# Kernel optimization log

Hardware: AMD Instinct MI355X
Metric: run time of the kernel (lower is better)

Reference implementation:

```python
import jax, jax.numpy as jnp
import numpy as np

IN_CH = 64
OUT_CH = 32
SCALE = 2
BLOCK = SCALE ** 3  # 8
N = 400000   # input sparse voxels (lines in pair_fwd)
M = 200000   # output sparse voxels


def setup_inputs() -> dict:
    key = jax.random.key(0)
    k1, k2, k3 = jax.random.split(key, 3)
    x_features = jax.random.normal(k1, (N, IN_CH), dtype=jnp.float32)
    # flat ParameterList: weights[i*BLOCK + j] is the (in_channels,) weight for
    # output channel i, kernel position j
    weights = jax.random.normal(k2, (BLOCK * OUT_CH, IN_CH), dtype=jnp.float32)
    # spconv pair_fwd: [kernel_volume, num_lines], -1 marks invalid mapping
    pair_fwd = jax.random.randint(k3, (BLOCK, N), -1, M)
    return {"x_features": x_features, "weights": weights,
            "pair_fwd": pair_fwd, "num_out": M}


def reference(x_features, weights, pair_fwd, num_out):
    block, n = pair_fwd.shape
    out_ch = weights.shape[0] // block
    # W[o, j, c] == weights_list[o*block + j]
    W = weights.reshape(out_ch, block, -1)
    # sequential VoxelShuffle then .view(-1) per block is identity on each
    # voxel's in_channels feature vector, so:
    # vals[j, n, o] = dot(W[o, j, :], x_features[n, :])
    vals = jnp.einsum('nc,ojc->jno', x_features, W)  # [block, N, out_ch]
    idx = pair_fwd.reshape(-1)                       # [block*N]
    # route invalid (-1) entries to a dummy trailing row
    safe = jnp.where(idx >= 0, idx, num_out)
    buf = jnp.zeros((num_out + 1, out_ch), dtype=vals.dtype)
    # original uses assignment (set) semantics into out_features
    buf = buf.at[safe].set(vals.reshape(block * n, out_ch))
    return buf[:num_out]
```

## Files before the change

kernel.cpp:

```cpp
#include <hip/hip_runtime.h>

#define IN_CH  64
#define OUT_CH 32
#define BLOCK  8

using short8 = __attribute__((ext_vector_type(8))) short;
using f32x4v = __attribute__((ext_vector_type(4))) float;


__global__ void k_prep(int4* __restrict__ argmax4, int n4, int* __restrict__ cur) {
    int i = blockIdx.x * 256 + threadIdx.x;
    if (i < 16) cur[i] = 0;
    if (i < n4) argmax4[i] = make_int4(-1, -1, -1, -1);
}

__global__ void k_scatter_range(const int* __restrict__ pair, int* __restrict__ argmax,
                                int N, int jhi, int jlo, int flip) {
    int n = blockIdx.x * 256 + threadIdx.x;
    if (n >= N) return;
    if (flip) n = N - 1 - n;
    for (int j = jhi; j >= jlo; --j) {
        int t = j * N + n;
        int m = pair[t];
        if (m >= 0 && argmax[m] < t)
            atomicMax(&argmax[m], t);
    }
}

__global__ void k_fill(const int* __restrict__ argmax, int* __restrict__ cur,
                       int* __restrict__ bm, int* __restrict__ bn, int M, int N) {
    __shared__ int h9[9];
    __shared__ int b9[9];
    if (threadIdx.x < 9) h9[threadIdx.x] = 0;
    __syncthreads();
    int m = blockIdx.x * 256 + threadIdx.x;
    int j = 9, n = 0, lo = 0;
    if (m < M) {
        int t = argmax[m];
        if (t >= 0) { j = (int)((unsigned)t / (unsigned)N); n = t - j * N; }
        else j = 8;
        lo = atomicAdd(&h9[j], 1);
    }
    __syncthreads();
    if (threadIdx.x < 9 && h9[threadIdx.x] > 0)
        b9[threadIdx.x] = atomicAdd(&cur[threadIdx.x], h9[threadIdx.x]);
    __syncthreads();
    if (m < M) {
        int pos = j * M + b9[j] + lo;
        bm[pos] = m;
        bn[pos] = n;
    }
}

__device__ __forceinline__ unsigned cvt_pk_bf16(float lo, float hi) {
    unsigned r;
    asm("v_cvt_pk_bf16_f32 %0, %1, %2" : "=v"(r) : "v"(lo), "v"(hi));
    return r;
}

__device__ __forceinline__ short8 pack8(float4 a, float4 b) {
    union { unsigned u[4]; short8 s; } p;
    p.u[0] = cvt_pk_bf16(a.x, a.y);
    p.u[1] = cvt_pk_bf16(a.z, a.w);
    p.u[2] = cvt_pk_bf16(b.x, b.y);
    p.u[3] = cvt_pk_bf16(b.z, b.w);
    return p.s;
}

__global__ __launch_bounds__(256, 4) void k_compute(
        const float* __restrict__ x, const float* __restrict__ w,
        const int* __restrict__ cnt, const int* __restrict__ bm,
        const int* __restrict__ bn, float* __restrict__ out, int M, int N) {
    const int lane = threadIdx.x & 63;
    const int r16  = lane & 15;
    const int kc   = lane >> 4;
    const int wv   = threadIdx.x >> 6;

    int T = blockIdx.x * 4 + wv;
    int j = 0, nrows = 0;
    for (; j < 9; ++j) {
        int c  = cnt[j];
        int nt = (c + 63) >> 6;
        if (T < nt) { nrows = min(64, c - T * 64); break; }
        T -= nt;
    }
    if (j >= 9) return;
    int base = j * M + T * 64;
    int jw = (j < 8) ? j : 0;

    short8 bf[2][2];
#pragma unroll
    for (int ot = 0; ot < 2; ++ot)
#pragma unroll
        for (int kk = 0; kk < 2; ++kk) {
            const float* wp = w + ((ot * 16 + r16) * BLOCK + jw) * IN_CH + kk * 32 + kc * 8;
            bf[ot][kk] = pack8(*(const float4*)wp, *(const float4*)(wp + 4));
        }

#pragma unroll
    for (int st = 0; st < 4; ++st) {
        if (st * 16 >= nrows) break;
        int lrow = st * 16 + r16;
        int n    = bn[base + ((lrow < nrows) ? lrow : 0)];
        const float* xp = x + (size_t)n * IN_CH + kc * 8;
        float4 x0 = *(const float4*)xp;
        float4 x1 = *(const float4*)(xp + 4);
        float4 x2 = *(const float4*)(xp + 32);
        float4 x3 = *(const float4*)(xp + 36);
        short8 a0 = pack8(x0, x1);
        short8 a1 = pack8(x2, x3);

        f32x4v acc0 = {0.f, 0.f, 0.f, 0.f};
        f32x4v acc1 = {0.f, 0.f, 0.f, 0.f};
        acc0 = __builtin_amdgcn_mfma_f32_16x16x32_bf16(a0, bf[0][0], acc0, 0, 0, 0);
        acc0 = __builtin_amdgcn_mfma_f32_16x16x32_bf16(a1, bf[0][1], acc0, 0, 0, 0);
        acc1 = __builtin_amdgcn_mfma_f32_16x16x32_bf16(a0, bf[1][0], acc1, 0, 0, 0);
        acc1 = __builtin_amdgcn_mfma_f32_16x16x32_bf16(a1, bf[1][1], acc1, 0, 0, 0);

        int4 m4 = *(const int4*)&bm[base + st * 16 + kc * 4];
        int ma[4] = {m4.x, m4.y, m4.z, m4.w};
#pragma unroll
        for (int q = 0; q < 4; ++q) {
            int grow = st * 16 + kc * 4 + q;
            if (grow < nrows) {
                size_t ro = (size_t)ma[q] * OUT_CH;
                float v0 = (j == 8) ? 0.f : acc0[q];
                float v1 = (j == 8) ? 0.f : acc1[q];
                out[ro + r16]      = v0;
                out[ro + 16 + r16] = v1;
            }
        }
    }
}

extern "C" void kernel_launch(void* const* d_in, const int* in_sizes, int n_in,
                              void* d_out, int out_size, void* d_ws, size_t ws_size,
                              hipStream_t stream) {
    const float* x    = (const float*)d_in[0];
    const float* w    = (const float*)d_in[1];
    const int*   pair = (const int*)d_in[2];
    int N = in_sizes[0] / IN_CH;
    int M = out_size / OUT_CH;

    char* ws     = (char*)d_ws;
    int*  cur    = (int*)ws;
    int*  argmax = (int*)(ws + 256);
    int*  bm     = (int*)(ws + 256 + (size_t)M * 4);
    int*  bn     = (int*)(ws + 256 + (size_t)M * 4 + (size_t)9 * M * 4);

    int n4 = M / 4;
    k_prep<<<(n4 + 255) / 256, 256, 0, stream>>>((int4*)argmax, n4, cur);

    int gN = (N + 255) / 256;
    k_scatter_range<<<gN, 256, 0, stream>>>(pair, argmax, N, 7, 7, 1);
    k_scatter_range<<<gN, 256, 0, stream>>>(pair, argmax, N, 6, 0, 0);

    k_fill<<<(M + 255) / 256, 256, 0, stream>>>(argmax, cur, bm, bn, M, N);

    int maxtiles = (M + 63) / 64 + 9;
    int blocks   = (maxtiles + 3) / 4;
    k_compute<<<blocks, 256, 0, stream>>>(x, w, cur, bm, bn, (float*)d_out, M, N);
}
```

Baseline: 91.30 us.

## Drop bucketing fill pass; compute directly per output row with masked per-kernel MFMAs

Removes the k_fill pass that bucketed output rows by kernel position, along with its bm/bn index arrays. The compute kernel now reads argmax per output row, decodes j and n, and runs MFMAs for every kernel position present in the wave, zero-masking rows that belong to other positions. All 8 weight slices are held in registers and the next x row is prefetched. The scatter kernels now read pair entries as int4 vectors. The change saves one launch plus the bm/bn writes and reads, and output stores become contiguous instead of scattered. In exchange it can issue up to 8x more MFMAs per tile, raises register pressure (launch bounds lowered to 2), and assumes N is divisible by 4.

```diff
diff --git a/kernel.cpp b/kernel.cpp
--- a/kernel.cpp
+++ b/kernel.cpp
@@ -8,47 +8,33 @@
 using f32x4v = __attribute__((ext_vector_type(4))) float;
 
 
-__global__ void k_prep(int4* __restrict__ argmax4, int n4, int* __restrict__ cur) {
+__global__ void k_prep(int4* __restrict__ argmax4, int n4) {
     int i = blockIdx.x * 256 + threadIdx.x;
-    if (i < 16) cur[i] = 0;
     if (i < n4) argmax4[i] = make_int4(-1, -1, -1, -1);
 }
 
-__global__ void k_scatter_range(const int* __restrict__ pair, int* __restrict__ argmax,
-                                int N, int jhi, int jlo, int flip) {
-    int n = blockIdx.x * 256 + threadIdx.x;
-    if (n >= N) return;
-    if (flip) n = N - 1 - n;
-    for (int j = jhi; j >= jlo; --j) {
-        int t = j * N + n;
-        int m = pair[t];
-        if (m >= 0 && argmax[m] < t)
-            atomicMax(&argmax[m], t);
-    }
+__global__ void k_scatter7(const int* __restrict__ pair, int* __restrict__ argmax, int N) {
+    int i = blockIdx.x * 256 + threadIdx.x;
+    int q = N / 4 - 1 - i;
+    if (q < 0) return;
+    int4 p = ((const int4*)(pair + 7 * N))[q];
+    int tb = 7 * N + q * 4;
+    if (p.w >= 0 && argmax[p.w] < tb + 3) atomicMax(&argmax[p.w], tb + 3);
+    if (p.z >= 0 && argmax[p.z] < tb + 2) atomicMax(&argmax[p.z], tb + 2);
+    if (p.y >= 0 && argmax[p.y] < tb + 1) atomicMax(&argmax[p.y], tb + 1);
+    if (p.x >= 0 && argmax[p.x] < tb)     atomicMax(&argmax[p.x], tb);
 }
 
-__global__ void k_fill(const int* __restrict__ argmax, int* __restrict__ cur,
-                       int* __restrict__ bm, int* __restrict__ bn, int M, int N) {
-    __shared__ int h9[9];
-    __shared__ int b9[9];
-    if (threadIdx.x < 9) h9[threadIdx.x] = 0;
-    __syncthreads();
-    int m = blockIdx.x * 256 + threadIdx.x;
-    int j = 9, n = 0, lo = 0;
-    if (m < M) {
-        int t = argmax[m];
-        if (t >= 0) { j = (int)((unsigned)t / (unsigned)N); n = t - j * N; }
-        else j = 8;
-        lo = atomicAdd(&h9[j], 1);
-    }
-    __syncthreads();
-    if (threadIdx.x < 9 && h9[threadIdx.x] > 0)
-        b9[threadIdx.x] = atomicAdd(&cur[threadIdx.x], h9[threadIdx.x]);
-    __syncthreads();
-    if (m < M) {
-        int pos = j * M + b9[j] + lo;
-        bm[pos] = m;
-        bn[pos] = n;
+__global__ void k_scatter_rest(const int* __restrict__ pair, int* __restrict__ argmax, int N) {
+    int i = blockIdx.x * 256 + threadIdx.x;
+    if (i >= N / 4) return;
+    for (int j = 6; j >= 0; --j) {
+        int4 p = ((const int4*)(pair + j * N))[i];
+        int tb = j * N + i * 4;
+        if (p.x >= 0 && argmax[p.x] < tb)     atomicMax(&argmax[p.x], tb);
+        if (p.y >= 0 && argmax[p.y] < tb + 1) atomicMax(&argmax[p.y], tb + 1);
+        if (p.z >= 0 && argmax[p.z] < tb + 2) atomicMax(&argmax[p.z], tb + 2);
+        if (p.w >= 0 && argmax[p.w] < tb + 3) atomicMax(&argmax[p.w], tb + 3);
     }
 }
 
@@ -67,67 +53,91 @@
     return p.s;
 }
 
-__global__ __launch_bounds__(256, 4) void k_compute(
+__global__ __launch_bounds__(256, 2) void k_compute(
         const float* __restrict__ x, const float* __restrict__ w,
-        const int* __restrict__ cnt, const int* __restrict__ bm,
-        const int* __restrict__ bn, float* __restrict__ out, int M, int N) {
+        const int* __restrict__ argmax, float* __restrict__ out,
+        int M, int N) {
     const int lane = threadIdx.x & 63;
     const int r16  = lane & 15;
     const int kc   = lane >> 4;
     const int wv   = threadIdx.x >> 6;
 
-    int T = blockIdx.x * 4 + wv;
-    int j = 0, nrows = 0;
-    for (; j < 9; ++j) {
-        int c  = cnt[j];
-        int nt = (c + 63) >> 6;
-        if (T < nt) { nrows = min(64, c - T * 64); break; }
-        T -= nt;
+    int base = (blockIdx.x * 4 + wv) * 64;
+    if (base >= M) return;
+
+    short8 bf[8][2][2];
+#pragma unroll
+    for (int j = 0; j < 8; ++j)
+#pragma unroll
+        for (int ot = 0; ot < 2; ++ot)
+#pragma unroll
+            for (int kk = 0; kk < 2; ++kk) {
+                const float* wp = w + ((ot * 16 + r16) * BLOCK + j) * IN_CH + kk * 32 + kc * 8;
+                bf[j][ot][kk] = pack8(*(const float4*)wp, *(const float4*)(wp + 4));
+            }
+
+    const int N1 = N, N2 = 2 * N, N4 = 4 * N;
+
+    int t_[4], j_[4], n_[4];
+#pragma unroll
+    for (int st = 0; st < 4; ++st) {
+        int row = base + st * 16 + r16;
+        t_[st] = (row < M) ? argmax[row] : -1;
     }
-    if (j >= 9) return;
-    int base = j * M + T * 64;
-    int jw = (j < 8) ? j : 0;
+#pragma unroll
+    for (int st = 0; st < 4; ++st) {
+        int v = t_[st], j = 0;
+        if (v >= N4) { j = 4;  v -= N4; }
+        if (v >= N2) { j += 2; v -= N2; }
+        if (v >= N1) { j += 1; v -= N1; }
+        bool ok = t_[st] >= 0;
+        j_[st] = ok ? j : 8;
+        n_[st] = ok ? v : 0;
+    }
 
-    short8 bf[2][2];
+    float4 xs[2][4];
+    {
+        const float* xp = x + (size_t)n_[0] * IN_CH + kc * 8;
+        xs[0][0] = *(const float4*)xp;       xs[0][1] = *(const float4*)(xp + 4);
+        xs[0][2] = *(const float4*)(xp + 32); xs[0][3] = *(const float4*)(xp + 36);
+    }
+
 #pragma unroll
-    for (int ot = 0; ot < 2; ++ot)
+    for (int st = 0; st < 4; ++st) {
+        const int cur = st & 1;
+        if (st < 3) {
+            const float* xp = x + (size_t)n_[st + 1] * IN_CH + kc * 8;
+            xs[cur ^ 1][0] = *(const float4*)xp;        xs[cur ^ 1][1] = *(const float4*)(xp + 4);
+            xs[cur ^ 1][2] = *(const float4*)(xp + 32); xs[cur ^ 1][3] = *(const float4*)(xp + 36);
+        }
+
+        short8 a0 = pack8(xs[cur][0], xs[cur][1]);
+        short8 a1 = pack8(xs[cur][2], xs[cur][3]);
+        const int jr = j_[st];
+        const short8 zz = (short8)0;
+
+        f32x4v acc0 = {0.f, 0.f, 0.f, 0.f};
+        f32x4v acc1 = {0.f, 0.f, 0.f, 0.f};
 #pragma unroll
-        for (int kk = 0; kk < 2; ++kk) {
-            const float* wp = w + ((ot * 16 + r16) * BLOCK + jw) * IN_CH + kk * 32 + kc * 8;
-            bf[ot][kk] = pack8(*(const float4*)wp, *(const float4*)(wp + 4));
+        for (int j = 0; j < 8; ++j) {
+            bool pj = (jr == j);
+            if (__ballot(pj)) {
+                short8 m0 = pj ? a0 : zz;
+                short8 m1 = pj ? a1 : zz;
+                acc0 = __builtin_amdgcn_mfma_f32_16x16x32_bf16(m0, bf[j][0][0], acc0, 0, 0, 0);
+                acc0 = __builtin_amdgcn_mfma_f32_16x16x32_bf16(m1, bf[j][0][1], acc0, 0, 0, 0);
+                acc1 = __builtin_amdgcn_mfma_f32_16x16x32_bf16(m0, bf[j][1][0], acc1, 0, 0, 0);
+                acc1 = __builtin_amdgcn_mfma_f32_16x16x32_bf16(m1, bf[j][1][1], acc1, 0, 0, 0);
+            }
         }
 
 #pragma unroll
-    for (int st = 0; st < 4; ++st) {
-        if (st * 16 >= nrows) break;
-        int lrow = st * 16 + r16;
-        int n    = bn[base + ((lrow < nrows) ? lrow : 0)];
-        const float* xp = x + (size_t)n * IN_CH + kc * 8;
-        float4 x0 = *(const float4*)xp;
-        float4 x1 = *(const float4*)(xp + 4);
-        float4 x2 = *(const float4*)(xp + 32);
-        float4 x3 = *(const float4*)(xp + 36);
-        short8 a0 = pack8(x0, x1);
-        short8 a1 = pack8(x2, x3);
-
-        f32x4v acc0 = {0.f, 0.f, 0.f, 0.f};
-        f32x4v acc1 = {0.f, 0.f, 0.f, 0.f};
-        acc0 = __builtin_amdgcn_mfma_f32_16x16x32_bf16(a0, bf[0][0], acc0, 0, 0, 0);
-        acc0 = __builtin_amdgcn_mfma_f32_16x16x32_bf16(a1, bf[0][1], acc0, 0, 0, 0);
-        acc1 = __builtin_amdgcn_mfma_f32_16x16x32_bf16(a0, bf[1][0], acc1, 0, 0, 0);
-        acc1 = __builtin_amdgcn_mfma_f32_16x16x32_bf16(a1, bf[1][1], acc1, 0, 0, 0);
-
-        int4 m4 = *(const int4*)&bm[base + st * 16 + kc * 4];
-        int ma[4] = {m4.x, m4.y, m4.z, m4.w};
-#pragma unroll
         for (int q = 0; q < 4; ++q) {
-            int grow = st * 16 + kc * 4 + q;
-            if (grow < nrows) {
-                size_t ro = (size_t)ma[q] * OUT_CH;
-                float v0 = (j == 8) ? 0.f : acc0[q];
-                float v1 = (j == 8) ? 0.f : acc1[q];
-                out[ro + r16]      = v0;
-                out[ro + 16 + r16] = v1;
+            int row = base + st * 16 + kc * 4 + q;
+            if (row < M) {
+                size_t ro = (size_t)row * OUT_CH;
+                out[ro + r16]      = acc0[q];
+                out[ro + 16 + r16] = acc1[q];
             }
         }
     }
@@ -142,22 +152,16 @@
     int N = in_sizes[0] / IN_CH;
     int M = out_size / OUT_CH;
 
-    char* ws     = (char*)d_ws;
-    int*  cur    = (int*)ws;
-    int*  argmax = (int*)(ws + 256);
-    int*  bm     = (int*)(ws + 256 + (size_t)M * 4);
-    int*  bn     = (int*)(ws + 256 + (size_t)M * 4 + (size_t)9 * M * 4);
+    int* argmax = (int*)d_ws;
 
     int n4 = M / 4;
-    k_prep<<<(n4 + 255) / 256, 256, 0, stream>>>((int4*)argmax, n4, cur);
+    k_prep<<<(n4 + 255) / 256, 256, 0, stream>>>((int4*)argmax, n4);
 
-    int gN = (N + 255) / 256;
-    k_scatter_range<<<gN, 256, 0, stream>>>(pair, argmax, N, 7, 7, 1);
-    k_scatter_range<<<gN, 256, 0, stream>>>(pair, argmax, N, 6, 0, 0);
+    int gq = (N / 4 + 255) / 256;
+    k_scatter7   <<<gq, 256, 0, stream>>>(pair, argmax, N);
+    k_scatter_rest<<<gq, 256, 0, stream>>>(pair, argmax, N);
 
-    k_fill<<<(M + 255) / 256, 256, 0, stream>>>(argmax, cur, bm, bn, M, N);
-
-    int maxtiles = (M + 63) / 64 + 9;
-    int blocks   = (maxtiles + 3) / 4;
-    k_compute<<<blocks, 256, 0, stream>>>(x, w, cur, bm, bn, (float*)d_out, M, N);
+    int waves  = (M + 63) / 64;
+    int blocks = (waves + 3) / 4;
+    k_compute<<<blocks, 256, 0, stream>>>(x, w, argmax, (float*)d_out, M, N);
 }
```

After: 111.9 us. 22.6% more time.

## Vectorize pair scatter with int4 loads and software-pipeline gathered feature loads

Applied to the files above, without the earlier changes.

The scatter kernels now read four pair entries per thread with int4 loads, processing each quad in reverse or forward order so the atomicMax last-writer logic is preserved. This cuts thread count and load instructions, but it assumes N is divisible by 4, and any tail entries are silently dropped. The compute kernel now prefetches all row indices and output indices up front. It also double-buffers the gathered x rows so the load for the next 16-row subtile overlaps the MFMA and stores of the current one. The cost is higher register pressure, which may reduce occupancy.

```diff
diff --git a/kernel.cpp b/kernel.cpp
--- a/kernel.cpp
+++ b/kernel.cpp
@@ -14,16 +14,28 @@
     if (i < n4) argmax4[i] = make_int4(-1, -1, -1, -1);
 }
 
-__global__ void k_scatter_range(const int* __restrict__ pair, int* __restrict__ argmax,
-                                int N, int jhi, int jlo, int flip) {
-    int n = blockIdx.x * 256 + threadIdx.x;
-    if (n >= N) return;
-    if (flip) n = N - 1 - n;
-    for (int j = jhi; j >= jlo; --j) {
-        int t = j * N + n;
-        int m = pair[t];
-        if (m >= 0 && argmax[m] < t)
-            atomicMax(&argmax[m], t);
+__global__ void k_scatter7(const int* __restrict__ pair, int* __restrict__ argmax, int N) {
+    int i = blockIdx.x * 256 + threadIdx.x;
+    int q = N / 4 - 1 - i;
+    if (q < 0) return;
+    int4 p = ((const int4*)(pair + 7 * N))[q];
+    int tb = 7 * N + q * 4;
+    if (p.w >= 0 && argmax[p.w] < tb + 3) atomicMax(&argmax[p.w], tb + 3);
+    if (p.z >= 0 && argmax[p.z] < tb + 2) atomicMax(&argmax[p.z], tb + 2);
+    if (p.y >= 0 && argmax[p.y] < tb + 1) atomicMax(&argmax[p.y], tb + 1);
+    if (p.x >= 0 && argmax[p.x] < tb)     atomicMax(&argmax[p.x], tb);
+}
+
+__global__ void k_scatter_rest(const int* __restrict__ pair, int* __restrict__ argmax, int N) {
+    int i = blockIdx.x * 256 + threadIdx.x;
+    if (i >= N / 4) return;
+    for (int j = 6; j >= 0; --j) {
+        int4 p = ((const int4*)(pair + j * N))[i];
+        int tb = j * N + i * 4;
+        if (p.x >= 0 && argmax[p.x] < tb)     atomicMax(&argmax[p.x], tb);
+        if (p.y >= 0 && argmax[p.y] < tb + 1) atomicMax(&argmax[p.y], tb + 1);
+        if (p.z >= 0 && argmax[p.z] < tb + 2) atomicMax(&argmax[p.z], tb + 2);
+        if (p.w >= 0 && argmax[p.w] < tb + 3) atomicMax(&argmax[p.w], tb + 3);
     }
 }
 
@@ -88,6 +100,17 @@
     int base = j * M + T * 64;
     int jw = (j < 8) ? j : 0;
 
+    int n_[4];
+    int4 m4_[4];
+#pragma unroll
+    for (int st = 0; st < 4; ++st) {
+        int lrow = st * 16 + r16;
+        n_[st] = bn[base + ((lrow < nrows) ? lrow : 0)];
+    }
+#pragma unroll
+    for (int st = 0; st < 4; ++st)
+        m4_[st] = *(const int4*)&bm[base + st * 16 + kc * 4];
+
     short8 bf[2][2];
 #pragma unroll
     for (int ot = 0; ot < 2; ++ot)
@@ -97,37 +120,43 @@
             bf[ot][kk] = pack8(*(const float4*)wp, *(const float4*)(wp + 4));
         }
 
+    float4 xs[2][4];
+    {
+        const float* xp = x + (size_t)n_[0] * IN_CH + kc * 8;
+        xs[0][0] = *(const float4*)xp;        xs[0][1] = *(const float4*)(xp + 4);
+        xs[0][2] = *(const float4*)(xp + 32); xs[0][3] = *(const float4*)(xp + 36);
+    }
+
 #pragma unroll
     for (int st = 0; st < 4; ++st) {
-        if (st * 16 >= nrows) break;
-        int lrow = st * 16 + r16;
-        int n    = bn[base + ((lrow < nrows) ? lrow : 0)];
-        const float* xp = x + (size_t)n * IN_CH + kc * 8;
-        float4 x0 = *(const float4*)xp;
-        float4 x1 = *(const float4*)(xp + 4);
-        float4 x2 = *(const float4*)(xp + 32);
-        float4 x3 = *(const float4*)(xp + 36);
-        short8 a0 = pack8(x0, x1);
-        short8 a1 = pack8(x2, x3);
+        const int cur2 = st & 1;
+        if (st < 3 && (st + 1) * 16 < nrows) {
+            const float* xp = x + (size_t)n_[st + 1] * IN_CH + kc * 8;
+            xs[cur2 ^ 1][0] = *(const float4*)xp;        xs[cur2 ^ 1][1] = *(const float4*)(xp + 4);
+            xs[cur2 ^ 1][2] = *(const float4*)(xp + 32); xs[cur2 ^ 1][3] = *(const float4*)(xp + 36);
+        }
+        if (st * 16 < nrows) {
+            short8 a0 = pack8(xs[cur2][0], xs[cur2][1]);
+            short8 a1 = pack8(xs[cur2][2], xs[cur2][3]);
 
-        f32x4v acc0 = {0.f, 0.f, 0.f, 0.f};
-        f32x4v acc1 = {0.f, 0.f, 0.f, 0.f};
-        acc0 = __builtin_amdgcn_mfma_f32_16x16x32_bf16(a0, bf[0][0], acc0, 0, 0, 0);
-        acc0 = __builtin_amdgcn_mfma_f32_16x16x32_bf16(a1, bf[0][1], acc0, 0, 0, 0);
-        acc1 = __builtin_amdgcn_mfma_f32_16x16x32_bf16(a0, bf[1][0], acc1, 0, 0, 0);
-        acc1 = __builtin_amdgcn_mfma_f32_16x16x32_bf16(a1, bf[1][1], acc1, 0, 0, 0);
+            f32x4v acc0 = {0.f, 0.f, 0.f, 0.f};
+            f32x4v acc1 = {0.f, 0.f, 0.f, 0.f};
+            acc0 = __builtin_amdgcn_mfma_f32_16x16x32_bf16(a0, bf[0][0], acc0, 0, 0, 0);
+            acc0 = __builtin_amdgcn_mfma_f32_16x16x32_bf16(a1, bf[0][1], acc0, 0, 0, 0);
+            acc1 = __builtin_amdgcn_mfma_f32_16x16x32_bf16(a0, bf[1][0], acc1, 0, 0, 0);
+            acc1 = __builtin_amdgcn_mfma_f32_16x16x32_bf16(a1, bf[1][1], acc1, 0, 0, 0);
 
-        int4 m4 = *(const int4*)&bm[base + st * 16 + kc * 4];
-        int ma[4] = {m4.x, m4.y, m4.z, m4.w};
+            int ma[4] = {m4_[st].x, m4_[st].y, m4_[st].z, m4_[st].w};
 #pragma unroll
-        for (int q = 0; q < 4; ++q) {
-            int grow = st * 16 + kc * 4 + q;
-            if (grow < nrows) {
-                size_t ro = (size_t)ma[q] * OUT_CH;
-                float v0 = (j == 8) ? 0.f : acc0[q];
-                float v1 = (j == 8) ? 0.f : acc1[q];
-                out[ro + r16]      = v0;
-                out[ro + 16 + r16] = v1;
+            for (int q = 0; q < 4; ++q) {
+                int grow = st * 16 + kc * 4 + q;
+                if (grow < nrows) {
+                    size_t ro = (size_t)ma[q] * OUT_CH;
+                    float v0 = (j == 8) ? 0.f : acc0[q];
+                    float v1 = (j == 8) ? 0.f : acc1[q];
+                    out[ro + r16]      = v0;
+                    out[ro + 16 + r16] = v1;
+                }
             }
         }
     }
@@ -151,9 +180,9 @@
     int n4 = M / 4;
     k_prep<<<(n4 + 255) / 256, 256, 0, stream>>>((int4*)argmax, n4, cur);
 
-    int gN = (N + 255) / 256;
-    k_scatter_range<<<gN, 256, 0, stream>>>(pair, argmax, N, 7, 7, 1);
-    k_scatter_range<<<gN, 256, 0, stream>>>(pair, argmax, N, 6, 0, 0);
+    int gq = (N / 4 + 255) / 256;
+    k_scatter7    <<<gq, 256, 0, stream>>>(pair, argmax, N);
+    k_scatter_rest<<<gq, 256, 0, stream>>>(pair, argmax, N);
 
     k_fill<<<(M + 255) / 256, 256, 0, stream>>>(argmax, cur, bm, bn, M, N);
 
```

Result: slower. 100.7 us (+10.3%).
